# Performance work log

Hardware: AMD Instinct MI355X
Metric: run time of the kernel (lower is better)

The kernel has to match this reference:

```python
import jax, jax.numpy as jnp
import numpy as np

L = 401            # cfg.n_anchor_bins
MIN_SEP = 2        # cfg.min_separation_bins
TARGET_ALPHA = 0.85
DIST_W, CTCF_W, COMP_W = 1.0, 0.5, 0.5
RATIO_TARGET = 1.5


def setup_inputs() -> dict:
    key = jax.random.key(0)
    k1, k2, k3 = jax.random.split(key, 3)
    B = 256
    contact_map = jax.random.normal(k1, (B, L, L), dtype=jnp.float32)
    compartment_logits = jax.random.normal(k2, (B, L, 2), dtype=jnp.float32)
    ctcf_orientation = (jax.random.randint(k3, (B, L), 0, 3) - 1).astype(jnp.int32)  # {-1,0,1}
    return {"contact_map": contact_map,
            "compartment_logits": compartment_logits,
            "ctcf_orientation": ctcf_orientation}


def reference(contact_map, compartment_logits, ctcf_orientation):
    B, Ld, _ = contact_map.shape
    dt = contact_map.dtype
    idx = jnp.arange(Ld)
    d = jnp.abs(idx[:, None] - idx[None, :])          # (L, L) int distance bins

    # ---- distance decay loss: one segment-reduce instead of a loop over bins ----
    bins = d.reshape(-1)                               # (L*L,)
    cm_sum = contact_map.sum(0).reshape(-1)            # sum over batch, flattened
    per_bin_sum = jax.ops.segment_sum(cm_sum, bins, num_segments=Ld)
    counts = jax.ops.segment_sum(jnp.ones_like(cm_sum), bins, num_segments=Ld)
    mean_c = per_bin_sum / (counts * B)                # mean contact per distance s
    s_vals = jnp.arange(Ld).astype(dt)
    valid = (idx >= MIN_SEP) & jnp.isfinite(mean_c) & (mean_c > 0)
    w = valid.astype(dt)
    n = w.sum()
    log_d = jnp.log(jnp.maximum(s_vals, 1.0))
    log_p = jnp.log(jnp.where(valid, mean_c, 1.0) + 1e-6)
    n_safe = jnp.maximum(n, 1.0)
    x_mean = (w * log_d).sum() / n_safe
    y_mean = (w * log_p).sum() / n_safe
    num = (w * (log_d - x_mean) * (log_p - y_mean)).sum()
    den = (w * (log_d - x_mean) ** 2).sum() + 1e-8
    slope = num / den
    dist_loss = jnp.where(n >= 5, (slope + TARGET_ALPHA) ** 2, jnp.zeros((), dt))

    # ---- CTCF convergence loss ----
    f = (ctcf_orientation == 1).astype(dt)             # (B, L)
    r = (ctcf_orientation == -1).astype(dt)
    convergent = f[:, :, None] * r[:, None, :]         # (B, L, L)
    any_c = (ctcf_orientation != 0).astype(dt)
    any_pair = any_c[:, :, None] * any_c[:, None, :]
    non_conv = any_pair * (1.0 - convergent)
    nc_sum = non_conv.sum()
    hinge = (jax.nn.relu(contact_map) * non_conv).sum() / (nc_sum + 1e-6)
    ctcf_loss = jnp.where(nc_sum < 1.0, jnp.zeros((), dt), hinge)

    # ---- compartment loss ----
    comp = jnp.argmax(jax.lax.stop_gradient(compartment_logits), axis=-1)  # (B, L)
    same = (comp[:, :, None] == comp[:, None, :]).astype(dt)               # (B, L, L)
    maskf = (d >= MIN_SEP).astype(dt)[None]                                # (1, L, L)
    within = (contact_map * same * maskf).sum() / jnp.maximum((same * maskf).sum(), 1.0)
    between = (contact_map * (1.0 - same) * maskf).sum() / jnp.maximum(((1.0 - same) * maskf).sum(), 1.0)
    ratio = within / (jnp.abs(between) + 1e-6)
    comp_loss = jax.nn.relu(RATIO_TARGET - ratio)

    total = DIST_W * dist_loss + CTCF_W * ctcf_loss + COMP_W * comp_loss
    return jnp.stack([dist_loss, ctcf_loss, comp_loss, total])
```

## Files before the change

### kernel.cpp

```cpp
#include <hip/hip_runtime.h>
#include <cmath>

#define LBINS 401
#define LL 160801
#define MIN_SEP 2
#define NBY 8
#define PSTRIDE 405

#define ACC_HANY  401
#define ACC_HCONV 402
#define ACC_SWM   403
#define ACC_SMM   404
#define ACCD_OFF  416
#define ZERO_FLOATS 420
#define PARTS_OFF 512

__global__ void zero_kernel(float* __restrict__ wsf) {
    int t = threadIdx.x;
    if (t < ZERO_FLOATS) wsf[t] = 0.0f;
}

__global__ __launch_bounds__(128)
void prep_kernel(const float* __restrict__ logits,
                 const int* __restrict__ ctcf,
                 double* __restrict__ accd) {
    int b = blockIdx.x;
    int tid = threadIdx.x;
    int n1 = 0, nf = 0, nr = 0, na = 0, adj = 0;
    const float* lg = logits + (size_t)b * LBINS * 2;
    const int*   ct = ctcf   + (size_t)b * LBINS;
    for (int l = tid; l < LBINS; l += 128) {
        int o = ct[l];
        int ci = (lg[2 * l + 1] > lg[2 * l]) ? 1 : 0;
        n1 += ci; nf += (o == 1); nr += (o == -1); na += (o != 0);
        if (l >= 1) {
            int cp = (lg[2 * (l - 1) + 1] > lg[2 * (l - 1)]) ? 1 : 0;
            adj += (ci == cp);
        }
    }
    #pragma unroll
    for (int off = 32; off > 0; off >>= 1) {
        n1 += __shfl_down(n1, off, 64);
        nf += __shfl_down(nf, off, 64);
        nr += __shfl_down(nr, off, 64);
        na += __shfl_down(na, off, 64);
        adj += __shfl_down(adj, off, 64);
    }
    __shared__ int ired[2][5];
    int w = tid >> 6;
    if ((tid & 63) == 0) {
        ired[w][0] = n1; ired[w][1] = nf; ired[w][2] = nr;
        ired[w][3] = na; ired[w][4] = adj;
    }
    __syncthreads();
    if (tid == 0) {
        int N1 = ired[0][0] + ired[1][0];
        int NF = ired[0][1] + ired[1][1];
        int NR = ired[0][2] + ired[1][2];
        int NA = ired[0][3] + ired[1][3];
        int AD = ired[0][4] + ired[1][4];
        int N0 = LBINS - N1;
        unsafeAtomicAdd(&accd[0], (double)NA * NA - (double)NF * NR);
        unsafeAtomicAdd(&accd[1],
            (double)N0 * N0 + (double)N1 * N1 - (double)LBINS - 2.0 * AD);
    }
}

__global__ __launch_bounds__(256)
void diag_kernel(const float* __restrict__ cm,
                 const float* __restrict__ logits,
                 const int* __restrict__ ctcf,
                 float* __restrict__ parts) {
    int b    = blockIdx.x;
    int band = blockIdx.y >> 1;
    int half = blockIdx.y & 1;
    int u    = threadIdx.x;
    int ka   = -400 + 256 * band;
    int k    = ka + u;

    __shared__ float4 colm[LBINS];
    __shared__ float4 rowm[LBINS];
    __shared__ float  lb[LBINS];
    __shared__ float  sred[4][4];

    const int*   ct = ctcf   + (size_t)b * LBINS;
    const float* lg = logits + (size_t)b * LBINS * 2;
    for (int t = u; t < LBINS; t += 256) {
        int o = ct[t];
        float any = (o != 0) ? 1.f : 0.f;
        float rev = (o == -1) ? 1.f : 0.f;
        float fwd = (o == 1) ? 1.f : 0.f;
        float cj  = (lg[2 * t + 1] > lg[2 * t]) ? 1.f : 0.f;
        colm[t] = make_float4(any, rev, cj, 0.f);
        rowm[t] = make_float4(any, fwd, 2.f * cj - 1.f, 1.f - cj);
        lb[t] = 0.f;
    }
    __syncthreads();

    int i_lo = max(0, -(ka + 255));
    int i_hi = min(LBINS, LBINS - ka);
    int len  = i_hi - i_lo;
    int mid  = i_lo + ((len + 1) >> 1);
    int is   = half ? mid : i_lo;
    int ie   = half ? i_hi : mid;

    const float* cmb = cm + (size_t)b * LL;
    float HA = 0.f, HC = 0.f, SW = 0.f, SM = 0.f;

    int i = is;
    for (; i + 4 <= ie; i += 4) {
        float  c[4];
        float4 cj4[4], rm4[4];
        #pragma unroll
        for (int q = 0; q < 4; ++q) {
            int ii = i + q;
            int j  = ii + k;
            int jc = min(max(j, 0), LBINS - 1);
            rm4[q] = rowm[ii];
            cj4[q] = colm[jc];
            float craw = cmb[(size_t)ii * LBINS + jc];
            c[q] = ((unsigned)j < (unsigned)LBINS) ? craw : 0.f;
        }
        #pragma unroll
        for (int q = 0; q < 4; ++q) {
            float cv = c[q];
            float rc = fmaxf(cv, 0.f);
            HA = fmaf(rm4[q].x * cj4[q].x, rc, HA);
            HC = fmaf(rm4[q].y * cj4[q].y, rc, HC);
            float sel = fmaf(rm4[q].z, cj4[q].z, rm4[q].w);
            SW = fmaf(sel, cv, SW);
            SM += cv;
        }
    }
    for (; i < ie; ++i) {
        int j  = i + k;
        int jc = min(max(j, 0), LBINS - 1);
        float4 rm = rowm[i];
        float4 cj = colm[jc];
        float craw = cmb[(size_t)i * LBINS + jc];
        float cv = ((unsigned)j < (unsigned)LBINS) ? craw : 0.f;
        float rc = fmaxf(cv, 0.f);
        HA = fmaf(rm.x * cj.x, rc, HA);
        HC = fmaf(rm.y * cj.y, rc, HC);
        float sel = fmaf(rm.z, cj.z, rm.w);
        SW = fmaf(sel, cv, SW);
        SM += cv;
    }

    int d = k < 0 ? -k : k; if (d > LBINS - 1) d = LBINS - 1;
    float dmask = (d >= MIN_SEP) ? 1.f : 0.f;
    atomicAdd(&lb[d], SM);
    float SWm = SW * dmask;
    float SMm = SM * dmask;

    #pragma unroll
    for (int off = 32; off > 0; off >>= 1) {
        HA  += __shfl_down(HA,  off, 64);
        HC  += __shfl_down(HC,  off, 64);
        SWm += __shfl_down(SWm, off, 64);
        SMm += __shfl_down(SMm, off, 64);
    }
    int w = u >> 6;
    if ((u & 63) == 0) {
        sred[w][0] = HA; sred[w][1] = HC; sred[w][2] = SWm; sred[w][3] = SMm;
    }
    __syncthreads();

    float* pout = parts + (size_t)(blockIdx.y * gridDim.x + blockIdx.x) * PSTRIDE;
    for (int t = u; t < LBINS; t += 256) pout[t] = lb[t];
    if (u == 0) {
        float a = 0.f, c2 = 0.f, s = 0.f, m = 0.f;
        #pragma unroll
        for (int q = 0; q < 4; ++q) {
            a += sred[q][0]; c2 += sred[q][1]; s += sred[q][2]; m += sred[q][3];
        }
        pout[401] = a; pout[402] = c2; pout[403] = s; pout[404] = m;
    }
}

__global__ __launch_bounds__(256)
void reduce_kernel(const float* __restrict__ parts,
                   float* __restrict__ accum, int npart) {
    int s = blockIdx.x;
    int u = threadIdx.x;
    float acc = 0.f;
    for (int p = u; p < npart; p += 256) acc += parts[(size_t)p * PSTRIDE + s];
    #pragma unroll
    for (int off = 32; off > 0; off >>= 1) acc += __shfl_down(acc, off, 64);
    __shared__ float r[4];
    if ((u & 63) == 0) r[u >> 6] = acc;
    __syncthreads();
    if (u == 0) accum[s] = r[0] + r[1] + r[2] + r[3];
}

__device__ double block_reduce_d(double v, double* buf) {
    int tid = threadIdx.x;
    buf[tid] = v;
    __syncthreads();
    for (int off = blockDim.x >> 1; off > 0; off >>= 1) {
        if (tid < off) buf[tid] += buf[tid + off];
        __syncthreads();
    }
    double r = buf[0];
    __syncthreads();
    return r;
}

__global__ __launch_bounds__(512)
void final_kernel(const float* __restrict__ accum,
                  const double* __restrict__ accd,
                  float* __restrict__ out, int B) {
    __shared__ double dred[512];
    int tid = threadIdx.x;

    double nc_sum   = accd[0];
    double same_cnt = accd[1];
    double total_maskf = (double)B * ((double)LL - 3.0 * LBINS + 2.0);
    double diff_cnt = total_maskf - same_cnt;

    float wgt = 0.f, x = 0.f, y = 0.f;
    if (tid < LBINS) {
        float cntB = ((tid == 0) ? (float)LBINS : 2.0f * (float)(LBINS - tid)) * (float)B;
        float mc = accum[tid] / cntB;
        int valid = (tid >= MIN_SEP) && __builtin_isfinite(mc) && (mc > 0.0f);
        wgt = valid ? 1.f : 0.f;
        x = logf(fmaxf((float)tid, 1.0f));
        y = logf((valid ? mc : 1.0f) + 1e-6f);
    }
    double n  = block_reduce_d((double)wgt, dred);
    double Sx = block_reduce_d((double)wgt * x, dred);
    double Sy = block_reduce_d((double)wgt * y, dred);
    double n_safe = fmax(n, 1.0);
    double xm = Sx / n_safe, ym = Sy / n_safe;
    double num = block_reduce_d((double)wgt * ((double)x - xm) * ((double)y - ym), dred);
    double den = block_reduce_d((double)wgt * ((double)x - xm) * ((double)x - xm), dred);

    if (tid == 0) {
        double slope = num / (den + 1e-8);
        float dist_loss = (n >= 5.0) ? (float)((slope + 0.85) * (slope + 0.85)) : 0.0f;

        float ncf = (float)nc_sum;
        float hinge = (accum[ACC_HANY] - accum[ACC_HCONV]) / (ncf + 1e-6f);
        float ctcf_loss = (ncf < 1.0f) ? 0.0f : hinge;

        float SW_m = accum[ACC_SWM];
        float SM_m = accum[ACC_SMM];
        float within  = SW_m / (float)fmax(same_cnt, 1.0);
        float between = (SM_m - SW_m) / (float)fmax(diff_cnt, 1.0);
        float ratio = within / (fabsf(between) + 1e-6f);
        float comp_loss = fmaxf(1.5f - ratio, 0.0f);

        float total = 1.0f * dist_loss + 0.5f * ctcf_loss + 0.5f * comp_loss;
        out[0] = dist_loss;
        out[1] = ctcf_loss;
        out[2] = comp_loss;
        out[3] = total;
    }
}

extern "C" void kernel_launch(void* const* d_in, const int* in_sizes, int n_in,
                              void* d_out, int out_size, void* d_ws, size_t ws_size,
                              hipStream_t stream) {
    const float* cm     = (const float*)d_in[0];
    const float* logits = (const float*)d_in[1];
    const int*   ctcf   = (const int*)d_in[2];
    float* out = (float*)d_out;

    int total = in_sizes[0];
    int B = total / LL;

    float*  wsf   = (float*)d_ws;
    float*  accum = wsf;
    double* accd  = (double*)(wsf + ACCD_OFF);
    float*  parts = wsf + PARTS_OFF;
    int npart = NBY * B;

    zero_kernel<<<1, 512, 0, stream>>>(wsf);
    prep_kernel<<<B, 128, 0, stream>>>(logits, ctcf, accd);
    diag_kernel<<<dim3(B, NBY), 256, 0, stream>>>(cm, logits, ctcf, parts);
    reduce_kernel<<<PSTRIDE, 256, 0, stream>>>(parts, accum, npart);
    final_kernel<<<1, 512, 0, stream>>>(accum, accd, out, B);
}
```

Measured before the change: 263.1 us.

## Use wrapped diagonals so each thread covers two distance bins, halving grid

Diagonals are now indexed by a cyclic offset k in [0,400], with a wrap at j>=L. Each thread walks one wrapped diagonal and splits its sums between distance k (unwrapped part) and L-k (wrapped part). This removes the clamped, masked-out iterations that the old band scheme spent outside the matrix, and halves the grid from 8 to 4 y-blocks. The unroll goes up to 8, and the zero kernel now clears only the double accumulators. The last k-group leaves most of its threads idle, and each iteration does a few more FMAs because of the split accumulators.

```diff
diff --git a/kernel.cpp b/kernel.cpp
--- a/kernel.cpp
+++ b/kernel.cpp
@@ -4,20 +4,18 @@
 #define LBINS 401
 #define LL 160801
 #define MIN_SEP 2
-#define NBY 8
 #define PSTRIDE 405
+#define UNR 8
 
 #define ACC_HANY  401
 #define ACC_HCONV 402
 #define ACC_SWM   403
 #define ACC_SMM   404
 #define ACCD_OFF  416
-#define ZERO_FLOATS 420
 #define PARTS_OFF 512
 
-__global__ void zero_kernel(float* __restrict__ wsf) {
-    int t = threadIdx.x;
-    if (t < ZERO_FLOATS) wsf[t] = 0.0f;
+__global__ void zero_kernel(double* __restrict__ accd) {
+    if (threadIdx.x < 2) accd[threadIdx.x] = 0.0;
 }
 
 __global__ __launch_bounds__(128)
@@ -71,12 +69,12 @@
                  const float* __restrict__ logits,
                  const int* __restrict__ ctcf,
                  float* __restrict__ parts) {
-    int b    = blockIdx.x;
-    int band = blockIdx.y >> 1;
-    int half = blockIdx.y & 1;
-    int u    = threadIdx.x;
-    int ka   = -400 + 256 * band;
-    int k    = ka + u;
+    int b      = blockIdx.x;
+    int ihalf  = blockIdx.y & 1;
+    int kgroup = blockIdx.y >> 1;
+    int u      = threadIdx.x;
+    int k      = kgroup * 256 + u;
+    bool active = (k < LBINS);
 
     __shared__ float4 colm[LBINS];
     __shared__ float4 rowm[LBINS];
@@ -97,61 +95,74 @@
     }
     __syncthreads();
 
-    int i_lo = max(0, -(ka + 255));
-    int i_hi = min(LBINS, LBINS - ka);
-    int len  = i_hi - i_lo;
-    int mid  = i_lo + ((len + 1) >> 1);
-    int is   = half ? mid : i_lo;
-    int ie   = half ? i_hi : mid;
+    int i0 = ihalf ? 201 : 0;
+    int ie = ihalf ? LBINS : 201;
 
     const float* cmb = cm + (size_t)b * LL;
-    float HA = 0.f, HC = 0.f, SW = 0.f, SM = 0.f;
-
-    int i = is;
-    for (; i + 4 <= ie; i += 4) {
-        float  c[4];
-        float4 cj4[4], rm4[4];
-        #pragma unroll
-        for (int q = 0; q < 4; ++q) {
-            int ii = i + q;
-            int j  = ii + k;
-            int jc = min(max(j, 0), LBINS - 1);
-            rm4[q] = rowm[ii];
-            cj4[q] = colm[jc];
-            float craw = cmb[(size_t)ii * LBINS + jc];
-            c[q] = ((unsigned)j < (unsigned)LBINS) ? craw : 0.f;
-        }
-        #pragma unroll
-        for (int q = 0; q < 4; ++q) {
-            float cv = c[q];
-            float rc = fmaxf(cv, 0.f);
-            HA = fmaf(rm4[q].x * cj4[q].x, rc, HA);
-            HC = fmaf(rm4[q].y * cj4[q].y, rc, HC);
-            float sel = fmaf(rm4[q].z, cj4[q].z, rm4[q].w);
-            SW = fmaf(sel, cv, SW);
-            SM += cv;
-        }
-    }
-    for (; i < ie; ++i) {
-        int j  = i + k;
-        int jc = min(max(j, 0), LBINS - 1);
-        float4 rm = rowm[i];
-        float4 cj = colm[jc];
-        float craw = cmb[(size_t)i * LBINS + jc];
-        float cv = ((unsigned)j < (unsigned)LBINS) ? craw : 0.f;
-        float rc = fmaxf(cv, 0.f);
-        HA = fmaf(rm.x * cj.x, rc, HA);
-        HC = fmaf(rm.y * cj.y, rc, HC);
-        float sel = fmaf(rm.z, cj.z, rm.w);
-        SW = fmaf(sel, cv, SW);
-        SM += cv;
-    }
-
-    int d = k < 0 ? -k : k; if (d > LBINS - 1) d = LBINS - 1;
-    float dmask = (d >= MIN_SEP) ? 1.f : 0.f;
-    atomicAdd(&lb[d], SM);
-    float SWm = SW * dmask;
-    float SMm = SM * dmask;
+    float HA = 0.f, HC = 0.f;
+    float SMk = 0.f, SMw = 0.f, SWk = 0.f, SWw = 0.f;
+
+    if (active) {
+        int i = i0;
+        for (; i + UNR <= ie; i += UNR) {
+            float  cv[UNR], sw[UNR];
+            float4 cj4[UNR], rm4[UNR];
+            #pragma unroll
+            for (int q = 0; q < UNR; ++q) {
+                int ii = i + q;
+                int j  = ii + k;
+                int wrapped = (j >= LBINS);
+                int jc = wrapped ? j - LBINS : j;
+                cv[q]  = cmb[(size_t)ii * LBINS + jc];
+                cj4[q] = colm[jc];
+                rm4[q] = rowm[ii];
+                sw[q]  = wrapped ? 1.f : 0.f;
+            }
+            #pragma unroll
+            for (int q = 0; q < UNR; ++q) {
+                float c  = cv[q];
+                float rc = fmaxf(c, 0.f);
+                HA = fmaf(rm4[q].x * cj4[q].x, rc, HA);
+                HC = fmaf(rm4[q].y * cj4[q].y, rc, HC);
+                float same = fmaf(rm4[q].z, cj4[q].z, rm4[q].w);
+                float sc = same * c;
+                float s = sw[q];
+                SWw = fmaf(s, sc, SWw);
+                SWk = fmaf(1.f - s, sc, SWk);
+                SMw = fmaf(s, c, SMw);
+                SMk = fmaf(1.f - s, c, SMk);
+            }
+        }
+        for (; i < ie; ++i) {
+            int j  = i + k;
+            int wrapped = (j >= LBINS);
+            int jc = wrapped ? j - LBINS : j;
+            float c = cmb[(size_t)i * LBINS + jc];
+            float4 cjv = colm[jc];
+            float4 rm  = rowm[i];
+            float s = wrapped ? 1.f : 0.f;
+            float rc = fmaxf(c, 0.f);
+            HA = fmaf(rm.x * cjv.x, rc, HA);
+            HC = fmaf(rm.y * cjv.y, rc, HC);
+            float same = fmaf(rm.z, cjv.z, rm.w);
+            float sc = same * c;
+            SWw = fmaf(s, sc, SWw);
+            SWk = fmaf(1.f - s, sc, SWk);
+            SMw = fmaf(s, c, SMw);
+            SMk = fmaf(1.f - s, c, SMk);
+        }
+    }
+
+    float SWm = 0.f, SMm = 0.f;
+    if (active) {
+        int dw = LBINS - k;
+        atomicAdd(&lb[k], SMk);
+        if (k > 0) atomicAdd(&lb[dw], SMw);
+        float mk = (k >= MIN_SEP) ? 1.f : 0.f;
+        float mw = (dw >= MIN_SEP) ? 1.f : 0.f;
+        SWm = SWk * mk + SWw * mw;
+        SMm = SMk * mk + SMw * mw;
+    }
 
     #pragma unroll
     for (int off = 32; off > 0; off >>= 1) {
@@ -273,11 +284,11 @@
     float*  accum = wsf;
     double* accd  = (double*)(wsf + ACCD_OFF);
     float*  parts = wsf + PARTS_OFF;
-    int npart = NBY * B;
-
-    zero_kernel<<<1, 512, 0, stream>>>(wsf);
+    int npart = 4 * B;
+
+    zero_kernel<<<1, 64, 0, stream>>>(accd);
     prep_kernel<<<B, 128, 0, stream>>>(logits, ctcf, accd);
-    diag_kernel<<<dim3(B, NBY), 256, 0, stream>>>(cm, logits, ctcf, parts);
+    diag_kernel<<<dim3(B, 4), 256, 0, stream>>>(cm, logits, ctcf, parts);
     reduce_kernel<<<PSTRIDE, 256, 0, stream>>>(parts, accum, npart);
     final_kernel<<<1, 512, 0, stream>>>(accum, accd, out, B);
 }
```

Result: faster. 256.3 us (-2.6%).
